# Performance work log

Measured on AMD Instinct MI355X. Metric: run time of the kernel, lower is better.

The kernel has to match this reference:

```python
import jax, jax.numpy as jnp
import numpy as np


def setup_inputs() -> dict:
    key = jax.random.key(0)
    kq, kk, kv = jax.random.split(key, 3)
    B, H, N, D = 2, 16, 2048, 128
    q = jax.random.normal(kq, (B, H, N, D), dtype=jnp.float32)
    k = jax.random.normal(kk, (B, H, N, D), dtype=jnp.float32)
    v = jax.random.normal(kv, (B, H, N, D), dtype=jnp.float32)
    return {"q": q, "k": k, "v": v, "num_sink": 4, "window_size": 1024}


def reference(q, k, v, num_sink, window_size):
    # Sink + sliding-window causal attention (single-device path of the SP wrapper).
    # Query i attends to key j iff j <= i AND (j < num_sink OR i - j < window_size).
    B, H, N, D = q.shape
    scale = 1.0 / np.sqrt(D).astype(np.float32)
    i = jnp.arange(N)[:, None]   # query positions
    j = jnp.arange(N)[None, :]   # key positions
    mask = (j <= i) & ((j < num_sink) | ((i - j) < window_size))  # [N, N]
    scores = jnp.einsum('bhid,bhjd->bhij', q, k) * scale          # [B,H,N,N]
    scores = jnp.where(mask, scores, jnp.finfo(scores.dtype).min)
    attn = jax.nn.softmax(scores, axis=-1)
    return jnp.einsum('bhij,bhjd->bhid', attn, v)
```

## Files before the change

kernel.cpp:

```cpp
#include <hip/hip_runtime.h>
#include <stdint.h>

#define NN 2048
#define DD 128
#define BHH 32
#define QT 64
#define KT 64

typedef short v8s __attribute__((ext_vector_type(8)));
typedef short v4s __attribute__((ext_vector_type(4)));
typedef float v4f __attribute__((ext_vector_type(4)));
typedef float v16f __attribute__((ext_vector_type(16)));
typedef unsigned int u32;
typedef u32 u32x2 __attribute__((ext_vector_type(2)));
typedef u32 u32x4 __attribute__((ext_vector_type(4)));

__device__ __forceinline__ unsigned short f2bf(float x) {
  unsigned u = __builtin_bit_cast(unsigned, x);
  u += 0x7fffu + ((u >> 16) & 1u);
  return (unsigned short)(u >> 16);
}

__device__ __forceinline__ v8s cvt8(const float* __restrict__ p) {
  v8s r;
#pragma unroll
  for (int j = 0; j < 8; j++) r[j] = (short)f2bf(p[j]);
  return r;
}

__device__ __forceinline__ u32 pk2(float a, float b) {
  u32 r;
  asm("v_cvt_pk_bf16_f32 %0, %1, %2" : "=v"(r) : "v"(a), "v"(b));
  return r;
}

__global__ __launch_bounds__(256) void prep(const float* __restrict__ K, const float* __restrict__ V,
                     unsigned short* __restrict__ Kb, unsigned short* __restrict__ Vt) {
  const int z = blockIdx.z;
  const int tid = threadIdx.x;
  if (z >= BHH) {
    const int bh = z - BHH;
    const int chunk = blockIdx.y * 32 + blockIdx.x;
    size_t base = (size_t)bh * NN * DD + (size_t)chunk * 4096 + (size_t)tid * 16;
    v4f f0 = *(const v4f*)(K + base);
    v4f f1 = *(const v4f*)(K + base + 4);
    v4f f2 = *(const v4f*)(K + base + 8);
    v4f f3 = *(const v4f*)(K + base + 12);
    u32x4 w0 = { pk2(f0[0], f0[1]), pk2(f0[2], f0[3]), pk2(f1[0], f1[1]), pk2(f1[2], f1[3]) };
    u32x4 w1 = { pk2(f2[0], f2[1]), pk2(f2[2], f2[3]), pk2(f3[0], f3[1]), pk2(f3[2], f3[3]) };
    *(u32x4*)(Kb + base) = w0;
    *(u32x4*)(Kb + base + 8) = w1;
    return;
  }
  __shared__ __align__(16) unsigned short t[64 * 68];
  const int bh = z;
  const int n0 = blockIdx.x * 64, d0 = blockIdx.y * 64;
  const int c16 = tid & 15, r4 = tid >> 4;
  const float* src = V + ((size_t)bh * NN + n0 + r4 * 4) * DD + d0 + c16 * 4;
  v4f f0 = *(const v4f*)(src);
  v4f f1 = *(const v4f*)(src + DD);
  v4f f2 = *(const v4f*)(src + 2 * DD);
  v4f f3 = *(const v4f*)(src + 3 * DD);
#pragma unroll
  for (int j = 0; j < 4; j++) {
    u32x2 w = { pk2(f0[j], f1[j]), pk2(f2[j], f3[j]) };
    *(u32x2*)(t + (c16 * 4 + j) * 68 + r4 * 4) = w;
  }
  __syncthreads();
  unsigned short* dst = Vt + ((size_t)bh * DD + d0) * NN + n0;
#pragma unroll
  for (int p = 0; p < 2; p++) {
    int d = p * 32 + (tid >> 3);
    int nc = (tid & 7) * 8;
    v4s x0 = *(const v4s*)(t + d * 68 + nc);
    v4s x1 = *(const v4s*)(t + d * 68 + nc + 4);
    v8s o = { x0[0], x0[1], x0[2], x0[3], x1[0], x1[1], x1[2], x1[3] };
    *(v8s*)(dst + (size_t)d * NN + nc) = o;
  }
}

template <bool PREPPED>
__global__ __launch_bounds__(128, 2) void attn(
    const float* __restrict__ Q,
    const float* __restrict__ Kf, const unsigned short* __restrict__ Kb,
    const unsigned short* __restrict__ Vt, const float* __restrict__ Vf,
    const int* __restrict__ nsp, const int* __restrict__ wsp,
    float* __restrict__ O) {
  const int ns = nsp[0], win = wsp[0];
  const int x = blockIdx.x;
  const int xcd = x & 7, slot = x >> 3;
  const int bh = xcd + 8 * (slot / 24);
  const int jobid = slot % 24;
  int qis[2], njobs;
  if (jobid < 16) { njobs = 1; qis[0] = 31 - jobid; qis[1] = 0; }
  else { int p = jobid - 16; njobs = 2; qis[0] = 15 - p; qis[1] = p; }

  const int tid = threadIdx.x;
  const int w = tid >> 6;
  const int l = tid & 63;
  const int m = l & 31;
  const int hi = l >> 5;
  const int rbase = 4 * hi;

  __shared__ __align__(16) unsigned short Kl[16 * 512];
  __shared__ __align__(16) unsigned short Vl[16 * 512];

  const float csc = 0.088388347648318447f * 1.4426950408889634f;

  const size_t kK = ((size_t)bh * NN + w * 32 + m) * DD + hi * 8;
  const unsigned short* vtb = Vt + (size_t)bh * DD * NN;

  auto mkpa = [&](float a0, float a1, float a2, float a3,
                  float b0, float b1, float b2, float b3) -> v8s {
    u32x2 r02 = __builtin_amdgcn_permlane32_swap(pk2(a0, a1), pk2(b0, b1), false, false);
    u32x2 r13 = __builtin_amdgcn_permlane32_swap(pk2(a2, a3), pk2(b2, b3), false, false);
    u32x4 pw = { r02[0], r13[0], r02[1], r13[1] };
    return __builtin_bit_cast(v8s, pw);
  };

  for (int ji = 0; ji < njobs; ji++) {
    const int q0 = qis[ji] * QT;
    const int qrow0w = q0 + w * 32;
    const int qi = qrow0w + m;

    v8s qf[8];
    {
      const float* qb = Q + ((size_t)bh * NN + qi) * DD + hi * 8;
#pragma unroll
      for (int kc = 0; kc < 8; kc++) {
        v8s r;
#pragma unroll
        for (int e = 0; e < 8; e++) r[e] = (short)f2bf(qb[kc * 16 + e] * csc);
        qf[kc] = r;
      }
    }

    float lsum = 0.f;
    v16f oa[4];
#pragma unroll
    for (int nc = 0; nc < 4; nc++) oa[nc] = (v16f)(0.f);

    const int wstart = q0 - win + 1;
    const bool sink16 = (wstart > KT - 1) && (ns <= 16);
    const int kb_lo = sink16 ? ((wstart >> 6) << 6) : 0;
    const int kb_hi = q0 + QT;

    v8s kst[8], vst[8];
    auto stage_load = [&](int kb) {
#pragma unroll
      for (int i = 0; i < 8; i++) {
        if constexpr (PREPPED) {
          kst[i] = *(const v8s*)(Kb + kK + (size_t)kb * DD + i * 16);
        } else {
          kst[i] = cvt8(Kf + kK + (size_t)kb * DD + i * 16);
        }
      }
#pragma unroll
      for (int i = 0; i < 8; i++) {
        const int kt = w * 2 + (i >> 2), nc = i & 3;
        if constexpr (PREPPED) {
          vst[i] = *(const v8s*)(vtb + ((size_t)nc * 32 + m) * NN + kb + kt * 16 + hi * 8);
        } else {
          v8s r;
#pragma unroll
          for (int e = 0; e < 8; e++)
            r[e] = (short)f2bf(Vf[((size_t)bh * NN + kb + kt * 16 + hi * 8 + e) * DD + nc * 32 + m]);
          vst[i] = r;
        }
      }
    };

    stage_load(kb_lo);

    if (sink16) {
      v8s kf0[8];
      const size_t g0 = ((size_t)bh * NN + m) * DD + hi * 8;
#pragma unroll
      for (int kc = 0; kc < 8; kc++)
        kf0[kc] = PREPPED ? *(const v8s*)(Kb + g0 + kc * 16) : cvt8(Kf + g0 + kc * 16);
      v16f s = (v16f)(0.f);
#pragma unroll
      for (int kc = 0; kc < 8; kc++)
        s = __builtin_amdgcn_mfma_f32_32x32x16_bf16(kf0[kc], qf[kc], s, 0, 0, 0);
#pragma unroll
      for (int reg = 0; reg < 16; reg++) {
        const int kj = (reg & 3) + 8 * (reg >> 2) + rbase;
        const bool valid = (kj < ns) && (kj <= qi);
        s[reg] = valid ? __builtin_amdgcn_exp2f(s[reg]) : 0.f;
        lsum += s[reg];
      }
      v8s pa = mkpa(s[0], s[1], s[2], s[3], s[4], s[5], s[6], s[7]);
#pragma unroll
      for (int nc = 0; nc < 4; nc++) {
        v8s vf;
        if constexpr (PREPPED) {
          vf = *(const v8s*)(vtb + ((size_t)nc * 32 + m) * NN + hi * 8);
        } else {
#pragma unroll
          for (int e = 0; e < 8; e++)
            vf[e] = (short)f2bf(Vf[((size_t)bh * NN + hi * 8 + e) * DD + nc * 32 + m]);
        }
        oa[nc] = __builtin_amdgcn_mfma_f32_32x32x16_bf16(pa, vf, oa[nc], 0, 0, 0);
      }
    }

    for (int kb = kb_lo; kb < kb_hi; kb += KT) {
      __syncthreads();
#pragma unroll
      for (int i = 0; i < 8; i++)
        *(v8s*)(Kl + (w * 8 + i) * 512 + l * 8) = kst[i];
#pragma unroll
      for (int i = 0; i < 8; i++)
        *(v8s*)(Vl + (w * 8 + i) * 512 + l * 8) = vst[i];
      __syncthreads();
      if (kb + KT < kb_hi) stage_load(kb + KT);

#pragma unroll
      for (int ct = 0; ct < 2; ct++) {
        v16f s = (v16f)(0.f);
        __builtin_amdgcn_s_setprio(1);
#pragma unroll
        for (int kc = 0; kc < 8; kc++) {
          v8s kfr = *(const v8s*)(Kl + (ct * 8 + kc) * 512 + l * 8);
          s = __builtin_amdgcn_mfma_f32_32x32x16_bf16(kfr, qf[kc], s, 0, 0, 0);
        }
        __builtin_amdgcn_s_setprio(0);

        const int kbct = kb + ct * 32;
        const bool full = (kbct + 31 <= qrow0w) && (kbct >= qrow0w + 32 - win);
        if (full) {
#pragma unroll
          for (int reg = 0; reg < 16; reg++) {
            s[reg] = __builtin_amdgcn_exp2f(s[reg]);
            lsum += s[reg];
          }
        } else {
#pragma unroll
          for (int reg = 0; reg < 16; reg++) {
            const int kj = kbct + (reg & 3) + 8 * (reg >> 2) + rbase;
            const bool valid = (kj <= qi) && ((kj < ns) || (qi - kj < win));
            s[reg] = valid ? __builtin_amdgcn_exp2f(s[reg]) : 0.f;
            lsum += s[reg];
          }
        }

        v8s pa0 = mkpa(s[0], s[1], s[2], s[3], s[4], s[5], s[6], s[7]);
        v8s pa1 = mkpa(s[8], s[9], s[10], s[11], s[12], s[13], s[14], s[15]);

        __builtin_amdgcn_s_setprio(1);
#pragma unroll
        for (int ktl = 0; ktl < 2; ktl++) {
          const v8s pf = ktl ? pa1 : pa0;
          const int kt = ct * 2 + ktl;
#pragma unroll
          for (int nc = 0; nc < 4; nc++) {
            v8s vfr = *(const v8s*)(Vl + (kt * 4 + nc) * 512 + l * 8);
            oa[nc] = __builtin_amdgcn_mfma_f32_32x32x16_bf16(pf, vfr, oa[nc], 0, 0, 0);
          }
        }
        __builtin_amdgcn_s_setprio(0);
      }
    }

    float lt = lsum + __shfl_xor(lsum, 32, 64);
    const float inv = 1.f / lt;
    float* ob = O + ((size_t)bh * NN + qrow0w) * DD;
#pragma unroll
    for (int reg = 0; reg < 16; reg++) {
      const int row = (reg & 3) + 8 * (reg >> 2) + rbase;
      const float iv = __shfl(inv, row, 64);
#pragma unroll
      for (int nc = 0; nc < 4; nc++)
        ob[(size_t)row * DD + nc * 32 + m] = oa[nc][reg] * iv;
    }
  }
}

extern "C" void kernel_launch(void* const* d_in, const int* in_sizes, int n_in,
                              void* d_out, int out_size, void* d_ws, size_t ws_size,
                              hipStream_t stream) {
  const float* q = (const float*)d_in[0];
  const float* k = (const float*)d_in[1];
  const float* v = (const float*)d_in[2];
  const int* nsp = (const int*)d_in[3];
  const int* wsp = (const int*)d_in[4];
  float* out = (float*)d_out;

  const size_t half = (size_t)BHH * NN * DD * sizeof(unsigned short);
  const int nblocks = BHH * 24;

  if (ws_size >= 2 * half) {
    unsigned short* kbf = (unsigned short*)d_ws;
    unsigned short* vt = (unsigned short*)((char*)d_ws + half);
    prep<<<dim3(32, 2, 2 * BHH), 256, 0, stream>>>(k, v, kbf, vt);
    attn<true><<<nblocks, 128, 0, stream>>>(q, k, kbf, vt, v, nsp, wsp, out);
  } else {
    attn<false><<<nblocks, 128, 0, stream>>>(q, k, nullptr, nullptr, v, nsp, wsp, out);
  }
}
```

Measured before the change: 196.2 us.

## Split KV tiles across two wave teams and prelayout V into MFMA fragments

Doubles the block to four waves organized as two teams that process alternating 64-key tiles for the same 64 query rows, then merges their partial outputs and row sums through shared memory. The prep kernel now writes V directly in MFMA B-fragment order, so V is read straight from global into registers instead of being staged through LDS. This is meant to add parallelism per query tile and cut LDS traffic for V. In exchange it adds a cross-team reduction, more registers for the per-ct V fragments, and an uneven split when the tile count is odd.

```diff
diff --git a/kernel.cpp b/kernel.cpp
--- a/kernel.cpp
+++ b/kernel.cpp
@@ -54,9 +54,9 @@
   }
   __shared__ __align__(16) unsigned short t[64 * 68];
   const int bh = z;
-  const int n0 = blockIdx.x * 64, d0 = blockIdx.y * 64;
+  const int n0b = blockIdx.x, d0b = blockIdx.y;
   const int c16 = tid & 15, r4 = tid >> 4;
-  const float* src = V + ((size_t)bh * NN + n0 + r4 * 4) * DD + d0 + c16 * 4;
+  const float* src = V + ((size_t)bh * NN + n0b * 64 + r4 * 4) * DD + d0b * 64 + c16 * 4;
   v4f f0 = *(const v4f*)(src);
   v4f f1 = *(const v4f*)(src + DD);
   v4f f2 = *(const v4f*)(src + 2 * DD);
@@ -67,23 +67,27 @@
     *(u32x2*)(t + (c16 * 4 + j) * 68 + r4 * 4) = w;
   }
   __syncthreads();
-  unsigned short* dst = Vt + ((size_t)bh * DD + d0) * NN + n0;
+  unsigned short* Vfb = Vt + (size_t)bh * (512u * 512);
 #pragma unroll
   for (int p = 0; p < 2; p++) {
-    int d = p * 32 + (tid >> 3);
-    int nc = (tid & 7) * 8;
-    v4s x0 = *(const v4s*)(t + d * 68 + nc);
-    v4s x1 = *(const v4s*)(t + d * 68 + nc + 4);
+    const int fid = p * 4 + (tid >> 6);
+    const int ktl = fid >> 1, ncl = fid & 1;
+    const int lane = tid & 63;
+    const int dloc = ncl * 32 + (lane & 31);
+    const int nloc = ktl * 16 + (lane >> 5) * 8;
+    v4s x0 = *(const v4s*)(t + dloc * 68 + nloc);
+    v4s x1 = *(const v4s*)(t + dloc * 68 + nloc + 4);
     v8s o = { x0[0], x0[1], x0[2], x0[3], x1[0], x1[1], x1[2], x1[3] };
-    *(v8s*)(dst + (size_t)d * NN + nc) = o;
+    const size_t fi = (size_t)(n0b * 4 + ktl) * 4 + (d0b * 2 + ncl);
+    *(v8s*)(Vfb + fi * 512 + (size_t)lane * 8) = o;
   }
 }
 
 template <bool PREPPED>
-__global__ __launch_bounds__(128, 2) void attn(
+__global__ __launch_bounds__(256, 2) void attn(
     const float* __restrict__ Q,
     const float* __restrict__ Kf, const unsigned short* __restrict__ Kb,
-    const unsigned short* __restrict__ Vt, const float* __restrict__ Vf,
+    const unsigned short* __restrict__ Vfr, const float* __restrict__ Vf,
     const int* __restrict__ nsp, const int* __restrict__ wsp,
     float* __restrict__ O) {
   const int ns = nsp[0], win = wsp[0];
@@ -96,19 +100,21 @@
   else { int p = jobid - 16; njobs = 2; qis[0] = 15 - p; qis[1] = p; }
 
   const int tid = threadIdx.x;
-  const int w = tid >> 6;
+  const int wave = tid >> 6;
+  const int team = wave >> 1;
+  const int wv = wave & 1;
   const int l = tid & 63;
   const int m = l & 31;
   const int hi = l >> 5;
   const int rbase = 4 * hi;
 
-  __shared__ __align__(16) unsigned short Kl[16 * 512];
-  __shared__ __align__(16) unsigned short Vl[16 * 512];
+  __shared__ __align__(16) unsigned short Kl[2][16 * 512];
+  __shared__ float Ls[128];
 
   const float csc = 0.088388347648318447f * 1.4426950408889634f;
 
-  const size_t kK = ((size_t)bh * NN + w * 32 + m) * DD + hi * 8;
-  const unsigned short* vtb = Vt + (size_t)bh * DD * NN;
+  const size_t kK = ((size_t)bh * NN + wv * 32 + m) * DD + hi * 8;
+  const unsigned short* Vfb = Vfr + (size_t)bh * (512u * 512);
 
   auto mkpa = [&](float a0, float a1, float a2, float a3,
                   float b0, float b1, float b2, float b3) -> v8s {
@@ -120,7 +126,7 @@
 
   for (int ji = 0; ji < njobs; ji++) {
     const int q0 = qis[ji] * QT;
-    const int qrow0w = q0 + w * 32;
+    const int qrow0w = q0 + wv * 32;
     const int qi = qrow0w + m;
 
     v8s qf[8];
@@ -144,35 +150,24 @@
     const bool sink16 = (wstart > KT - 1) && (ns <= 16);
     const int kb_lo = sink16 ? ((wstart >> 6) << 6) : 0;
     const int kb_hi = q0 + QT;
-
-    v8s kst[8], vst[8];
+    const int ntiles = (kb_hi - kb_lo) >> 6;
+    const int T = (ntiles + 1) >> 1;
+
+    v8s kst[8];
     auto stage_load = [&](int kb) {
 #pragma unroll
       for (int i = 0; i < 8; i++) {
-        if constexpr (PREPPED) {
+        if constexpr (PREPPED)
           kst[i] = *(const v8s*)(Kb + kK + (size_t)kb * DD + i * 16);
-        } else {
+        else
           kst[i] = cvt8(Kf + kK + (size_t)kb * DD + i * 16);
-        }
-      }
-#pragma unroll
-      for (int i = 0; i < 8; i++) {
-        const int kt = w * 2 + (i >> 2), nc = i & 3;
-        if constexpr (PREPPED) {
-          vst[i] = *(const v8s*)(vtb + ((size_t)nc * 32 + m) * NN + kb + kt * 16 + hi * 8);
-        } else {
-          v8s r;
-#pragma unroll
-          for (int e = 0; e < 8; e++)
-            r[e] = (short)f2bf(Vf[((size_t)bh * NN + kb + kt * 16 + hi * 8 + e) * DD + nc * 32 + m]);
-          vst[i] = r;
-        }
       }
     };
 
-    stage_load(kb_lo);
-
-    if (sink16) {
+    const int kb0 = kb_lo + team * KT;
+    if (kb0 < kb_hi) stage_load(kb0);
+
+    if (sink16 && team == 1) {
       v8s kf0[8];
       const size_t g0 = ((size_t)bh * NN + m) * DD + hi * 8;
 #pragma unroll
@@ -187,14 +182,15 @@
         const int kj = (reg & 3) + 8 * (reg >> 2) + rbase;
         const bool valid = (kj < ns) && (kj <= qi);
         s[reg] = valid ? __builtin_amdgcn_exp2f(s[reg]) : 0.f;
-        lsum += s[reg];
-      }
+      }
+      lsum += (((s[0] + s[1]) + (s[2] + s[3])) + ((s[4] + s[5]) + (s[6] + s[7])))
+            + (((s[8] + s[9]) + (s[10] + s[11])) + ((s[12] + s[13]) + (s[14] + s[15])));
       v8s pa = mkpa(s[0], s[1], s[2], s[3], s[4], s[5], s[6], s[7]);
 #pragma unroll
       for (int nc = 0; nc < 4; nc++) {
         v8s vf;
         if constexpr (PREPPED) {
-          vf = *(const v8s*)(vtb + ((size_t)nc * 32 + m) * NN + hi * 8);
+          vf = *(const v8s*)(Vfb + (size_t)nc * 512 + (size_t)l * 8);
         } else {
 #pragma unroll
           for (int e = 0; e < 8; e++)
@@ -204,24 +200,43 @@
       }
     }
 
-    for (int kb = kb_lo; kb < kb_hi; kb += KT) {
+    for (int it = 0; it < T; ++it) {
+      const int kb = kb_lo + (2 * it + team) * KT;
+      const bool act = kb < kb_hi;
       __syncthreads();
-#pragma unroll
-      for (int i = 0; i < 8; i++)
-        *(v8s*)(Kl + (w * 8 + i) * 512 + l * 8) = kst[i];
-#pragma unroll
-      for (int i = 0; i < 8; i++)
-        *(v8s*)(Vl + (w * 8 + i) * 512 + l * 8) = vst[i];
+      if (act) {
+#pragma unroll
+        for (int i = 0; i < 8; i++)
+          *(v8s*)(Kl[team] + (wv * 8 + i) * 512 + l * 8) = kst[i];
+      }
       __syncthreads();
-      if (kb + KT < kb_hi) stage_load(kb + KT);
+      if (!act) continue;
+      if (kb + 2 * KT < kb_hi) stage_load(kb + 2 * KT);
 
 #pragma unroll
       for (int ct = 0; ct < 2; ct++) {
+        v8s vf[8];
+        if constexpr (PREPPED) {
+#pragma unroll
+          for (int i = 0; i < 8; i++) {
+            const int ktl = i >> 2, nc = i & 3;
+            vf[i] = *(const v8s*)(Vfb + ((size_t)((kb >> 4) + ct * 2 + ktl) * 4 + nc) * 512 + (size_t)l * 8);
+          }
+        } else {
+#pragma unroll
+          for (int i = 0; i < 8; i++) {
+            const int ktl = i >> 2, nc = i & 3;
+#pragma unroll
+            for (int e = 0; e < 8; e++)
+              vf[i][e] = (short)f2bf(Vf[((size_t)bh * NN + kb + (ct * 2 + ktl) * 16 + hi * 8 + e) * DD + nc * 32 + m]);
+          }
+        }
+
         v16f s = (v16f)(0.f);
         __builtin_amdgcn_s_setprio(1);
 #pragma unroll
         for (int kc = 0; kc < 8; kc++) {
-          v8s kfr = *(const v8s*)(Kl + (ct * 8 + kc) * 512 + l * 8);
+          v8s kfr = *(const v8s*)(Kl[team] + (ct * 8 + kc) * 512 + l * 8);
           s = __builtin_amdgcn_mfma_f32_32x32x16_bf16(kfr, qf[kc], s, 0, 0, 0);
         }
         __builtin_amdgcn_s_setprio(0);
@@ -230,19 +245,17 @@
         const bool full = (kbct + 31 <= qrow0w) && (kbct >= qrow0w + 32 - win);
         if (full) {
 #pragma unroll
-          for (int reg = 0; reg < 16; reg++) {
-            s[reg] = __builtin_amdgcn_exp2f(s[reg]);
-            lsum += s[reg];
-          }
+          for (int reg = 0; reg < 16; reg++) s[reg] = __builtin_amdgcn_exp2f(s[reg]);
         } else {
 #pragma unroll
           for (int reg = 0; reg < 16; reg++) {
             const int kj = kbct + (reg & 3) + 8 * (reg >> 2) + rbase;
             const bool valid = (kj <= qi) && ((kj < ns) || (qi - kj < win));
             s[reg] = valid ? __builtin_amdgcn_exp2f(s[reg]) : 0.f;
-            lsum += s[reg];
           }
         }
+        lsum += (((s[0] + s[1]) + (s[2] + s[3])) + ((s[4] + s[5]) + (s[6] + s[7])))
+              + (((s[8] + s[9]) + (s[10] + s[11])) + ((s[12] + s[13]) + (s[14] + s[15])));
 
         v8s pa0 = mkpa(s[0], s[1], s[2], s[3], s[4], s[5], s[6], s[7]);
         v8s pa1 = mkpa(s[8], s[9], s[10], s[11], s[12], s[13], s[14], s[15]);
@@ -251,27 +264,43 @@
 #pragma unroll
         for (int ktl = 0; ktl < 2; ktl++) {
           const v8s pf = ktl ? pa1 : pa0;
-          const int kt = ct * 2 + ktl;
-#pragma unroll
-          for (int nc = 0; nc < 4; nc++) {
-            v8s vfr = *(const v8s*)(Vl + (kt * 4 + nc) * 512 + l * 8);
-            oa[nc] = __builtin_amdgcn_mfma_f32_32x32x16_bf16(pf, vfr, oa[nc], 0, 0, 0);
-          }
+#pragma unroll
+          for (int nc = 0; nc < 4; nc++)
+            oa[nc] = __builtin_amdgcn_mfma_f32_32x32x16_bf16(pf, vf[ktl * 4 + nc], oa[nc], 0, 0, 0);
         }
         __builtin_amdgcn_s_setprio(0);
       }
     }
 
-    float lt = lsum + __shfl_xor(lsum, 32, 64);
-    const float inv = 1.f / lt;
-    float* ob = O + ((size_t)bh * NN + qrow0w) * DD;
-#pragma unroll
-    for (int reg = 0; reg < 16; reg++) {
-      const int row = (reg & 3) + 8 * (reg >> 2) + rbase;
-      const float iv = __shfl(inv, row, 64);
+    __syncthreads();
+    float* ex = (float*)&Kl[0][0];
+    if (team == 1) {
 #pragma unroll
       for (int nc = 0; nc < 4; nc++)
-        ob[(size_t)row * DD + nc * 32 + m] = oa[nc][reg] * iv;
+#pragma unroll
+        for (int reg = 0; reg < 16; reg++)
+          ex[(nc * 16 + reg) * 128 + wv * 64 + l] = oa[nc][reg];
+      Ls[wv * 64 + l] = lsum;
+    }
+    __syncthreads();
+    if (team == 0) {
+#pragma unroll
+      for (int nc = 0; nc < 4; nc++)
+#pragma unroll
+        for (int reg = 0; reg < 16; reg++)
+          oa[nc][reg] += ex[(nc * 16 + reg) * 128 + wv * 64 + l];
+      float lt = lsum + Ls[wv * 64 + l];
+      lt += __shfl_xor(lt, 32, 64);
+      const float inv = 1.f / lt;
+      float* ob = O + ((size_t)bh * NN + qrow0w) * DD;
+#pragma unroll
+      for (int reg = 0; reg < 16; reg++) {
+        const int row = (reg & 3) + 8 * (reg >> 2) + rbase;
+        const float iv = __shfl(inv, row, 64);
+#pragma unroll
+        for (int nc = 0; nc < 4; nc++)
+          ob[(size_t)row * DD + nc * 32 + m] = oa[nc][reg] * iv;
+      }
     }
   }
 }
@@ -291,10 +320,10 @@
 
   if (ws_size >= 2 * half) {
     unsigned short* kbf = (unsigned short*)d_ws;
-    unsigned short* vt = (unsigned short*)((char*)d_ws + half);
-    prep<<<dim3(32, 2, 2 * BHH), 256, 0, stream>>>(k, v, kbf, vt);
-    attn<true><<<nblocks, 128, 0, stream>>>(q, k, kbf, vt, v, nsp, wsp, out);
+    unsigned short* vfrag = (unsigned short*)((char*)d_ws + half);
+    prep<<<dim3(32, 2, 2 * BHH), 256, 0, stream>>>(k, v, kbf, vfrag);
+    attn<true><<<nblocks, 256, 0, stream>>>(q, k, kbf, vfrag, v, nsp, wsp, out);
   } else {
-    attn<false><<<nblocks, 128, 0, stream>>>(q, k, nullptr, nullptr, v, nsp, wsp, out);
-  }
-}
+    attn<false><<<nblocks, 256, 0, stream>>>(q, k, nullptr, nullptr, v, nsp, wsp, out);
+  }
+}
```

Measured after the change: 209.0 us. +6.5%, slower.
